# Kernel optimization log

Measured on AMD Instinct MI355X. Metric: run time of the kernel, lower is better.

Reference implementation:

```python
import jax, jax.numpy as jnp
import numpy as np

OT_REG = 0.1
OT_ITERS = 10
LN_EPS = 1e-5


def layernorm(x, g, b):
    m = jnp.mean(x, axis=-1, keepdims=True)
    v = jnp.mean((x - m) ** 2, axis=-1, keepdims=True)
    return (x - m) * jax.lax.rsqrt(v + LN_EPS) * g + b


def sinkhorn(C, epsilon, iters):
    # standard Sinkhorn: kernel exp(C/eps), alternate row/col normalization
    Q = jnp.exp(C / epsilon)  # [Na,B,La,Lb]
    def body(_, Q):
        Q = Q / jnp.sum(Q, axis=-1, keepdims=True)
        Q = Q / jnp.sum(Q, axis=-2, keepdims=True)
        return Q
    return jax.lax.fori_loop(0, iters, body, Q)


def setup_inputs() -> dict:
    key = jax.random.key(0)
    ks = jax.random.split(key, 16)
    Na, La, B, Lb, Din, H = 32, 32, 64, 32, 768, 768
    s = 0.02
    return {
        "entity_cls": jax.random.normal(ks[0], (Na, Din), jnp.float32),
        "entity_tokens": jax.random.normal(ks[1], (Na, La, Din), jnp.float32),
        "mention_cls": jax.random.normal(ks[2], (B, Din), jnp.float32),
        "mention_tokens": jax.random.normal(ks[3], (B, Lb, Din), jnp.float32),
        "Wq": jax.random.normal(ks[4], (Din, H), jnp.float32) * s,
        "bq": jnp.zeros((H,), jnp.float32),
        "Wk": jax.random.normal(ks[5], (Din, H), jnp.float32) * s,
        "bk": jnp.zeros((H,), jnp.float32),
        "Wv": jax.random.normal(ks[6], (Din, H), jnp.float32) * s,
        "bv": jnp.zeros((H,), jnp.float32),
        "ln1_g": jnp.ones((H,), jnp.float32),
        "ln1_b": jnp.zeros((H,), jnp.float32),
        "Wcls": jax.random.normal(ks[7], (Din, H), jnp.float32) * s,
        "bcls": jnp.zeros((H,), jnp.float32),
        "Wsp": jax.random.normal(ks[8], (H, 1), jnp.float32) * s,
        "bsp": jnp.zeros((1,), jnp.float32),
        "ln2_g": jnp.ones((H,), jnp.float32),
        "ln2_b": jnp.zeros((H,), jnp.float32),
    }


def reference(entity_cls, entity_tokens, mention_cls, mention_tokens,
              Wq, bq, Wk, bk, Wv, bv, ln1_g, ln1_b,
              Wcls, bcls, Wsp, bsp, ln2_g, ln2_b):
    # projections
    q = entity_tokens @ Wq + bq      # [Na,La,H]
    k = mention_tokens @ Wk + bk     # [B,Lb,H]
    v = mention_tokens @ Wv + bv     # [B,Lb,H]

    # cross-batch cosine similarity: [Na,B,La,Lb]
    qn = q / jnp.maximum(jnp.linalg.norm(q, axis=-1, keepdims=True), 1e-8)
    kn = k / jnp.maximum(jnp.linalg.norm(k, axis=-1, keepdims=True), 1e-8)
    C = jnp.einsum('aid,bjd->abij', qn, kn)

    # Sinkhorn on detached cost (torch uses C.detach())
    T = sinkhorn(jax.lax.stop_gradient(C), OT_REG, OT_ITERS)
    # F.normalize(dim=-1): L2 normalize last dim
    T = T / jnp.maximum(jnp.linalg.norm(T, axis=-1, keepdims=True), 1e-12)

    # attention + residual + layernorm: [Na,B,La,H]
    attended = jnp.einsum('abij,bjd->abid', T, v) + q[:, None, :, :]
    attended = layernorm(attended, ln1_g, ln1_b)

    # softpool over token dim (-2)
    w = jax.nn.softmax(attended @ Wsp + bsp, axis=-2)   # [Na,B,La,1]
    pooled = jnp.sum(attended * w, axis=-2)             # [Na,B,H]
    context = layernorm(pooled, ln2_g, ln2_b)

    # matching scores
    ecls = entity_cls @ Wcls + bcls                     # [Na,H]
    g2l = jnp.sum(ecls[:, None, :] * context, axis=-1)  # [Na,B]
    g2l = g2l.T                                         # [B,Na]
    g2g = mention_cls @ entity_cls.T                    # [B,Na]
    return (g2l + g2g) * 0.5
```

## Files before the change

### kernel.cpp

```cpp
#include <hip/hip_runtime.h>
#include <math.h>


typedef __attribute__((ext_vector_type(8))) short bfrag8;
typedef __attribute__((ext_vector_type(4))) float f32x4;

__device__ __forceinline__ unsigned short f2bf(float x) {
  union { float f; unsigned u; } v; v.f = x;
  unsigned r = v.u + 0x7fffu + ((v.u >> 16) & 1u);
  return (unsigned short)(r >> 16);
}

__global__ __launch_bounds__(256) void prep_kernel(
    const float* __restrict__ a0, const float* __restrict__ a1, const float* __restrict__ a2,
    unsigned short* __restrict__ o0, unsigned short* __restrict__ o1, unsigned short* __restrict__ o2,
    float* __restrict__ nrm,
    const float* __restrict__ W0, const float* __restrict__ W1,
    const float* __restrict__ W2, const float* __restrict__ W3,
    unsigned short* __restrict__ T0, unsigned short* __restrict__ T1,
    unsigned short* __restrict__ T2, unsigned short* __restrict__ T3) {
  __shared__ float t[32][33];
  int bx = blockIdx.x;
  if (bx < 2331) {
    if (bx < 2328) {
      const float* in; unsigned short* out; int i, n4;
      if (bx < 768)       { in = a0; out = o0; i = bx * 256 + threadIdx.x;          n4 = 196608; }
      else if (bx < 2304) { in = a1; out = o1; i = (bx - 768) * 256 + threadIdx.x;  n4 = 393216; }
      else                { in = a2; out = o2; i = (bx - 2304) * 256 + threadIdx.x; n4 = 6144; }
      if (i >= n4) return;
      float4 f = ((const float4*)in)[i];
      ushort4 o;
      o.x = f2bf(f.x); o.y = f2bf(f.y); o.z = f2bf(f.z); o.w = f2bf(f.w);
      ((ushort4*)out)[i] = o;
    } else {
      int i = (bx - 2328) * 256 + threadIdx.x;
      if (i < 768) ((float4*)nrm)[i] = make_float4(0.f, 0.f, 0.f, 0.f);
    }
    return;
  }
  int idx = bx - 2331;
  int z = idx / 576, r2 = idx % 576;
  int tby = r2 / 24, tbx = r2 % 24;
  const float* W = (z == 0) ? W0 : (z == 1) ? W1 : (z == 2) ? W2 : W3;
  unsigned short* O = (z == 0) ? T0 : (z == 1) ? T1 : (z == 2) ? T2 : T3;
  const int gx = tbx * 32, gy = tby * 32;
  const int tx = threadIdx.x & 31, ty = threadIdx.x >> 5;
#pragma unroll
  for (int u = 0; u < 4; ++u) {
    int row = ty + u * 8;
    t[row][tx] = W[(size_t)(gy + row) * 768 + gx + tx];
  }
  __syncthreads();
#pragma unroll
  for (int u = 0; u < 4; ++u) {
    int row = ty + u * 8;
    O[(size_t)(gx + row) * 768 + gy + tx] = f2bf(t[tx][row]);
  }
}

__global__ __launch_bounds__(256) void proj_gemm_kernel(
    const unsigned short* __restrict__ Ae, const unsigned short* __restrict__ Am,
    const unsigned short* __restrict__ Acls,
    const unsigned short* __restrict__ WqT, const unsigned short* __restrict__ WkT,
    const unsigned short* __restrict__ WvT, const unsigned short* __restrict__ WclsT,
    const float* __restrict__ bq, const float* __restrict__ bk,
    const float* __restrict__ bv, const float* __restrict__ bcls,
    unsigned short* __restrict__ qb, unsigned short* __restrict__ qT,
    unsigned short* __restrict__ kb, unsigned short* __restrict__ vT,
    float* __restrict__ ecls, float* __restrict__ iq_sq, float* __restrict__ ik_sq) {
  const int z = blockIdx.z;
  const int M = (z == 0) ? 1024 : (z == 3) ? 32 : 2048;
  const int bm = blockIdx.y * 128;
  if (bm >= M) return;
  const unsigned short* A = (z == 3) ? Acls : (z == 0) ? Ae : Am;
  const unsigned short* B = (z == 0) ? WqT : (z == 1) ? WkT : (z == 2) ? WvT : WclsT;
  const float* bias = (z == 0) ? bq : (z == 1) ? bk : (z == 2) ? bv : bcls;

  __shared__ unsigned short As[128 * 64];
  __shared__ unsigned short Bs[128 * 64];
  const int t = threadIdx.x;
  const int bn = blockIdx.x * 128;
  const int l = t & 63, w = t >> 6;
  const int wm = w & 1, wn = w >> 1;

  f32x4 acc[4][4];
#pragma unroll
  for (int mi = 0; mi < 4; ++mi)
#pragma unroll
    for (int nj = 0; nj < 4; ++nj) { f32x4 zz = {0.f, 0.f, 0.f, 0.f}; acc[mi][nj] = zz; }

  for (int k0 = 0; k0 < 768; k0 += 64) {
    __syncthreads();
#pragma unroll
    for (int u = 0; u < 4; ++u) {
      int c = t + u * 256;
      int row = c >> 3, kc = c & 7;
      int gm = bm + row; gm = gm < M ? gm : M - 1;
      int4 av = *(const int4*)(A + (size_t)gm * 768 + k0 + kc * 8);
      *(int4*)(As + row * 64 + ((kc ^ (row & 7)) * 8)) = av;
      int4 bv4 = *(const int4*)(B + (size_t)(bn + row) * 768 + k0 + kc * 8);
      *(int4*)(Bs + row * 64 + ((kc ^ (row & 7)) * 8)) = bv4;
    }
    __syncthreads();
#pragma unroll
    for (int kk = 0; kk < 2; ++kk) {
      bfrag8 af[4], bf[4];
      const int kc = kk * 4 + (l >> 4);
#pragma unroll
      for (int mi = 0; mi < 4; ++mi) {
        int arow = wm * 64 + mi * 16 + (l & 15);
        af[mi] = *(const bfrag8*)(As + arow * 64 + ((kc ^ (arow & 7)) * 8));
      }
#pragma unroll
      for (int nj = 0; nj < 4; ++nj) {
        int brow = wn * 64 + nj * 16 + (l & 15);
        bf[nj] = *(const bfrag8*)(Bs + brow * 64 + ((kc ^ (brow & 7)) * 8));
      }
#pragma unroll
      for (int mi = 0; mi < 4; ++mi)
#pragma unroll
        for (int nj = 0; nj < 4; ++nj)
          acc[mi][nj] = __builtin_amdgcn_mfma_f32_16x16x32_bf16(af[mi], bf[nj], acc[mi][nj], 0, 0, 0);
    }
  }

  const int col = l & 15, rq = l >> 4;
  float p[4][4] = {};
#pragma unroll
  for (int mi = 0; mi < 4; ++mi) {
#pragma unroll
    for (int nj = 0; nj < 4; ++nj) {
      int gn = bn + wn * 64 + nj * 16 + col;
      float bs = bias[gn];
#pragma unroll
      for (int r = 0; r < 4; ++r) {
        int gm = bm + wm * 64 + mi * 16 + rq * 4 + r;
        if (gm >= M) continue;
        float val = acc[mi][nj][r] + bs;
        if (z < 2) p[mi][r] += val * val;
        unsigned short bfv = f2bf(val);
        if (z == 0) {
          qb[(size_t)gm * 768 + gn] = bfv;
          int at = gm >> 5, j = gm & 31;
          qT[((size_t)at * 768 + gn) * 32 + j] = bfv;
        } else if (z == 1) kb[(size_t)gm * 768 + gn] = bfv;
        else if (z == 2) {
          int bb = gm >> 5, j = gm & 31;
          vT[((size_t)bb * 768 + gn) * 32 + j] = bfv;
        } else ecls[(size_t)gm * 768 + gn] = val;
      }
    }
  }
  if (z < 2) {
    float* nrm = (z == 0) ? iq_sq : ik_sq;
#pragma unroll
    for (int mi = 0; mi < 4; ++mi)
#pragma unroll
      for (int r = 0; r < 4; ++r) {
        float s = p[mi][r];
        s += __shfl_xor(s, 1); s += __shfl_xor(s, 2);
        s += __shfl_xor(s, 4); s += __shfl_xor(s, 8);
        if (col == 0) {
          int gm = bm + wm * 64 + mi * 16 + rq * 4 + r;
          atomicAdd(&nrm[gm], s);
        }
      }
  }
}

__global__ __launch_bounds__(256) void cos_attn_kernel(
    const unsigned short* __restrict__ qb, const unsigned short* __restrict__ kb,
    const float* __restrict__ iq_sq, const float* __restrict__ ik_sq,
    const unsigned short* __restrict__ qT,
    const unsigned short* __restrict__ vT,
    const float* __restrict__ ln1_g, const float* __restrict__ ln1_b,
    const float* __restrict__ Wsp, const float* __restrict__ bsp,
    const float* __restrict__ ln2_g, const float* __restrict__ ln2_b,
    const float* __restrict__ ecls,
    const float* __restrict__ entity_cls, const float* __restrict__ mention_cls,
    float* __restrict__ out) {
  __shared__ unsigned short vLds[2 * 768 * 32];
  __shared__ __align__(16) unsigned short scratch[12288];
  __shared__ float gabLds[4 * 768];
  __shared__ float gwLds[768];
  __shared__ float ldsIq[128], ldsIk[64];
  __shared__ float red[40];

  unsigned short* As = scratch;
  unsigned short* Bs = scratch + 8192;
  unsigned short* Tlds = scratch;

  const int t = threadIdx.x;
  const int l = t & 63, w = t >> 6;
  const int bm = blockIdx.y * 128, bn = blockIdx.x * 64;
  const int wm = w & 1, wn = w >> 1;
  const int cg = l & 15, rq = l >> 4;

  {
    float sgw = 0.f, sbw = 0.f, sga[4] = {}, sba[4] = {};
#pragma unroll
    for (int cc = 0; cc < 3; ++cc) {
      int h = t + cc * 256;
      float g1 = ln1_g[h], b1 = ln1_b[h], wsp = Wsp[h];
      float g2 = ln2_g[h], b2 = ln2_b[h];
      float gw = g1 * wsp;
      gwLds[h] = gw;
      sgw += gw; sbw += b1 * wsp;
#pragma unroll
      for (int aa = 0; aa < 4; ++aa) {
        float ec = ecls[(size_t)((blockIdx.y << 2) + aa) * 768 + h];
        float gab = g2 * ec;
        gabLds[aa * 768 + h] = gab;
        sga[aa] += gab; sba[aa] += b2 * ec;
      }
    }
#pragma unroll
    for (int m = 1; m < 64; m <<= 1) {
      sgw += __shfl_xor(sgw, m); sbw += __shfl_xor(sbw, m);
#pragma unroll
      for (int aa = 0; aa < 4; ++aa) { sga[aa] += __shfl_xor(sga[aa], m); sba[aa] += __shfl_xor(sba[aa], m); }
    }
    if (l == 0) {
      red[w * 10 + 0] = sgw; red[w * 10 + 1] = sbw;
#pragma unroll
      for (int aa = 0; aa < 4; ++aa) { red[w * 10 + 2 + aa] = sga[aa]; red[w * 10 + 6 + aa] = sba[aa]; }
    }
  }
  if (t < 128) ldsIq[t] = iq_sq[bm + t];
  else if (t < 192) ldsIk[t - 128] = ik_sq[bn + t - 128];

  const int4* vsrc = (const int4*)(vT + (size_t)(blockIdx.x * 2) * 768 * 32);
  int4* vdst = (int4*)vLds;

  f32x4 acc[4][2];
#pragma unroll
  for (int mi = 0; mi < 4; ++mi)
#pragma unroll
    for (int nj = 0; nj < 2; ++nj) { f32x4 zz = {0.f, 0.f, 0.f, 0.f}; acc[mi][nj] = zz; }

  for (int k0 = 0, s = 0; k0 < 768; k0 += 64, ++s) {
    __syncthreads();
#pragma unroll
    for (int u = 0; u < 4; ++u) {
      int c = t + u * 256;
      int row = c >> 3, kc = c & 7;
      int4 av = *(const int4*)(qb + (size_t)(bm + row) * 768 + k0 + kc * 8);
      *(int4*)(As + row * 64 + ((kc ^ (row & 7)) * 8)) = av;
    }
#pragma unroll
    for (int u = 0; u < 2; ++u) {
      int c = t + u * 256;
      int row = c >> 3, kc = c & 7;
      int4 bv4 = *(const int4*)(kb + (size_t)(bn + row) * 768 + k0 + kc * 8);
      *(int4*)(Bs + row * 64 + ((kc ^ (row & 7)) * 8)) = bv4;
    }
    vdst[t + (2 * s) * 256] = vsrc[t + (2 * s) * 256];
    vdst[t + (2 * s + 1) * 256] = vsrc[t + (2 * s + 1) * 256];
    __syncthreads();
#pragma unroll
    for (int kk = 0; kk < 2; ++kk) {
      bfrag8 af[4], bf[2];
      const int kc = kk * 4 + rq;
#pragma unroll
      for (int mi = 0; mi < 4; ++mi) {
        int arow = wm * 64 + mi * 16 + cg;
        af[mi] = *(const bfrag8*)(As + arow * 64 + ((kc ^ (arow & 7)) * 8));
      }
#pragma unroll
      for (int nj = 0; nj < 2; ++nj) {
        int brow = wn * 32 + nj * 16 + cg;
        bf[nj] = *(const bfrag8*)(Bs + brow * 64 + ((kc ^ (brow & 7)) * 8));
      }
#pragma unroll
      for (int mi = 0; mi < 4; ++mi)
#pragma unroll
        for (int nj = 0; nj < 2; ++nj)
          acc[mi][nj] = __builtin_amdgcn_mfma_f32_16x16x32_bf16(af[mi], bf[nj], acc[mi][nj], 0, 0, 0);
    }
  }

  float irow[4][4], icol[2];
#pragma unroll
  for (int mi = 0; mi < 4; ++mi)
#pragma unroll
    for (int r = 0; r < 4; ++r) {
      float sv = ldsIq[wm * 64 + mi * 16 + rq * 4 + r];
      irow[mi][r] = 1.0f / fmaxf(sqrtf(sv), 1e-8f);
    }
#pragma unroll
  for (int nj = 0; nj < 2; ++nj) {
    float sv = ldsIk[wn * 32 + nj * 16 + cg];
    icol[nj] = 1.0f / fmaxf(sqrtf(sv), 1e-8f);
  }
#pragma unroll
  for (int mi = 0; mi < 4; ++mi)
#pragma unroll
    for (int nj = 0; nj < 2; ++nj)
#pragma unroll
      for (int r = 0; r < 4; ++r)
        acc[mi][nj][r] = __expf(acc[mi][nj][r] * irow[mi][r] * icol[nj] * 10.0f);

  for (int it = 0; it < 10; ++it) {
#pragma unroll
    for (int mi = 0; mi < 4; ++mi)
#pragma unroll
      for (int r = 0; r < 4; ++r) {
        float rs = acc[mi][0][r] + acc[mi][1][r];
        rs += __shfl_xor(rs, 1); rs += __shfl_xor(rs, 2);
        rs += __shfl_xor(rs, 4); rs += __shfl_xor(rs, 8);
        float rinv = __builtin_amdgcn_rcpf(rs);
        acc[mi][0][r] *= rinv; acc[mi][1][r] *= rinv;
      }
#pragma unroll
    for (int ta = 0; ta < 2; ++ta)
#pragma unroll
      for (int nj = 0; nj < 2; ++nj) {
        float cs = acc[2 * ta][nj][0] + acc[2 * ta][nj][1] + acc[2 * ta][nj][2] + acc[2 * ta][nj][3]
                 + acc[2 * ta + 1][nj][0] + acc[2 * ta + 1][nj][1] + acc[2 * ta + 1][nj][2] + acc[2 * ta + 1][nj][3];
        cs += __shfl_xor(cs, 16); cs += __shfl_xor(cs, 32);
        float cinv = __builtin_amdgcn_rcpf(cs);
#pragma unroll
        for (int mi2 = 0; mi2 < 2; ++mi2)
#pragma unroll
          for (int r = 0; r < 4; ++r) acc[2 * ta + mi2][nj][r] *= cinv;
      }
  }

#pragma unroll
  for (int mi = 0; mi < 4; ++mi)
#pragma unroll
    for (int r = 0; r < 4; ++r) {
      float ss = acc[mi][0][r] * acc[mi][0][r] + acc[mi][1][r] * acc[mi][1][r];
      ss += __shfl_xor(ss, 1); ss += __shfl_xor(ss, 2);
      ss += __shfl_xor(ss, 4); ss += __shfl_xor(ss, 8);
      float tinv = 1.0f / fmaxf(sqrtf(ss), 1e-12f);
      acc[mi][0][r] *= tinv; acc[mi][1][r] *= tinv;
    }

  __syncthreads();
#pragma unroll
  for (int mi = 0; mi < 4; ++mi) {
    const int a_loc = wm * 2 + (mi >> 1);
    unsigned short* base = Tlds + ((wn * 4 + a_loc) << 10);
    const int ri0 = (mi & 1) * 16 + rq * 4;
#pragma unroll
    for (int nj = 0; nj < 2; ++nj)
#pragma unroll
      for (int r = 0; r < 4; ++r)
        base[(ri0 + r) * 32 + nj * 16 + cg] = f2bf(acc[mi][nj][r]);
  }
  __syncthreads();

  const int bl = w & 1, ah = w >> 1;
  const int b_g = (blockIdx.x << 1) + bl;
  const unsigned short* vbase = vLds + bl * 24576;

  float sgw_f = 0.f, sbw_f = 0.f, sga_f[2] = {}, sba_f[2] = {};
#pragma unroll
  for (int wv = 0; wv < 4; ++wv) {
    sgw_f += red[wv * 10 + 0]; sbw_f += red[wv * 10 + 1];
    sga_f[0] += red[wv * 10 + 2 + ah * 2]; sga_f[1] += red[wv * 10 + 3 + ah * 2];
    sba_f[0] += red[wv * 10 + 6 + ah * 2]; sba_f[1] += red[wv * 10 + 7 + ah * 2];
  }
  sbw_f += bsp[0];

  bfrag8 af[2][2], afI[2];
  const unsigned short* qTa[2];
#pragma unroll
  for (int ap = 0; ap < 2; ++ap) {
    const int a_local = ah * 2 + ap;
    qTa[ap] = qT + (size_t)((blockIdx.y << 2) + a_local) * 24576;
    const unsigned short* Tp = Tlds + ((bl * 4 + a_local) << 10);
#pragma unroll
    for (int mi = 0; mi < 2; ++mi)
      af[ap][mi] = *(const bfrag8*)(Tp + (mi * 16 + cg) * 32 + rq * 8);
  }
#pragma unroll
  for (int mi = 0; mi < 2; ++mi) {
    int row = mi * 16 + cg;
    bfrag8 fI;
#pragma unroll
    for (int u = 0; u < 8; ++u) fI[u] = (row == rq * 8 + u) ? (short)0x3F80 : (short)0;
    afI[mi] = fI;
  }

  float s1[2][2][4] = {}, s2[2][2][4] = {}, a1[2][2][4] = {};
#pragma unroll 2
  for (int nj = 0; nj < 48; ++nj) {
    int h = nj * 16 + cg;
    bfrag8 vf = *(const bfrag8*)(vbase + h * 32 + rq * 8);
    float gw = gwLds[h];
#pragma unroll
    for (int ap = 0; ap < 2; ++ap) {
      bfrag8 qf = *(const bfrag8*)(qTa[ap] + (size_t)h * 32 + rq * 8);
#pragma unroll
      for (int mi = 0; mi < 2; ++mi) {
        f32x4 zz = {0.f, 0.f, 0.f, 0.f};
        f32x4 p = __builtin_amdgcn_mfma_f32_16x16x32_bf16(af[ap][mi], vf, zz, 0, 0, 0);
        f32x4 x4 = __builtin_amdgcn_mfma_f32_16x16x32_bf16(afI[mi], qf, p, 0, 0, 0);
#pragma unroll
        for (int r = 0; r < 4; ++r) {
          float x = x4[r];
          s1[ap][mi][r] += x; s2[ap][mi][r] += x * x; a1[ap][mi][r] += x * gw;
        }
      }
    }
  }
#pragma unroll
  for (int m = 1; m < 16; m <<= 1)
#pragma unroll
    for (int ap = 0; ap < 2; ++ap)
#pragma unroll
      for (int mi = 0; mi < 2; ++mi)
#pragma unroll
        for (int r = 0; r < 4; ++r) {
          s1[ap][mi][r] += __shfl_xor(s1[ap][mi][r], m);
          s2[ap][mi][r] += __shfl_xor(s2[ap][mi][r], m);
          a1[ap][mi][r] += __shfl_xor(a1[ap][mi][r], m);
        }

  float uu[2][2][4], c0[2];
#pragma unroll
  for (int ap = 0; ap < 2; ++ap) {
    float mean[2][4], rstd[2][4], logit[2][4];
#pragma unroll
    for (int mi = 0; mi < 2; ++mi)
#pragma unroll
      for (int r = 0; r < 4; ++r) {
        float m1 = s1[ap][mi][r] * (1.0f / 768.0f);
        float var = s2[ap][mi][r] * (1.0f / 768.0f) - m1 * m1;
        float rs = rsqrtf(var + 1e-5f);
        mean[mi][r] = m1; rstd[mi][r] = rs;
        logit[mi][r] = rs * (a1[ap][mi][r] - m1 * sgw_f) + sbw_f;
      }
    float mx = logit[0][0];
#pragma unroll
    for (int mi = 0; mi < 2; ++mi)
#pragma unroll
      for (int r = 0; r < 4; ++r) mx = fmaxf(mx, logit[mi][r]);
    mx = fmaxf(mx, __shfl_xor(mx, 16)); mx = fmaxf(mx, __shfl_xor(mx, 32));
    float se = 0.f, ee[2][4];
#pragma unroll
    for (int mi = 0; mi < 2; ++mi)
#pragma unroll
      for (int r = 0; r < 4; ++r) { ee[mi][r] = __expf(logit[mi][r] - mx); se += ee[mi][r]; }
    se += __shfl_xor(se, 16); se += __shfl_xor(se, 32);
    const float sinv = __builtin_amdgcn_rcpf(se);
    float c0a = 0.f;
#pragma unroll
    for (int mi = 0; mi < 2; ++mi)
#pragma unroll
      for (int r = 0; r < 4; ++r) {
        uu[ap][mi][r] = ee[mi][r] * sinv * rstd[mi][r];
        c0a += uu[ap][mi][r] * mean[mi][r];
      }
    c0a += __shfl_xor(c0a, 16); c0a += __shfl_xor(c0a, 32);
    c0[ap] = c0a;
  }

  float ps[2] = {}, pq[2] = {}, spc[2] = {};
#pragma unroll 2
  for (int nj = 0; nj < 48; ++nj) {
    int h = nj * 16 + cg;
    bfrag8 vf = *(const bfrag8*)(vbase + h * 32 + rq * 8);
    float g1h = ln1_g[h], b1h = ln1_b[h];
#pragma unroll
    for (int ap = 0; ap < 2; ++ap) {
      bfrag8 qf = *(const bfrag8*)(qTa[ap] + (size_t)h * 32 + rq * 8);
      float pp = 0.f;
#pragma unroll
      for (int mi = 0; mi < 2; ++mi) {
        f32x4 zz = {0.f, 0.f, 0.f, 0.f};
        f32x4 p = __builtin_amdgcn_mfma_f32_16x16x32_bf16(af[ap][mi], vf, zz, 0, 0, 0);
        f32x4 x4 = __builtin_amdgcn_mfma_f32_16x16x32_bf16(afI[mi], qf, p, 0, 0, 0);
#pragma unroll
        for (int r = 0; r < 4; ++r) pp += uu[ap][mi][r] * x4[r];
      }
      pp += __shfl_xor(pp, 16); pp += __shfl_xor(pp, 32);
      float pooled = g1h * (pp - c0[ap]) + b1h;
      ps[ap] += pooled; pq[ap] += pooled * pooled;
      spc[ap] += pooled * gabLds[(ah * 2 + ap) * 768 + h];
    }
  }

#pragma unroll
  for (int ap = 0; ap < 2; ++ap) {
#pragma unroll
    for (int m = 1; m < 16; m <<= 1) {
      ps[ap] += __shfl_xor(ps[ap], m); pq[ap] += __shfl_xor(pq[ap], m); spc[ap] += __shfl_xor(spc[ap], m);
    }
    const float m2 = ps[ap] * (1.0f / 768.0f);
    const float var2 = pq[ap] * (1.0f / 768.0f) - m2 * m2;
    const float rs2 = rsqrtf(var2 + 1e-5f);
    const int a_g = (blockIdx.y << 2) + ah * 2 + ap;
    const float* ea = entity_cls + (size_t)a_g * 768;
    const float* mb = mention_cls + (size_t)b_g * 768;
    float sg = 0.f;
#pragma unroll
    for (int u = 0; u < 12; ++u) sg += mb[l * 12 + u] * ea[l * 12 + u];
#pragma unroll
    for (int m = 1; m < 64; m <<= 1) sg += __shfl_xor(sg, m);
    float tot = rs2 * (spc[ap] - m2 * sga_f[ap]) + sba_f[ap] + sg;
    if (l == 0) out[b_g * 32 + a_g] = 0.5f * tot;
  }
}

extern "C" void kernel_launch(void* const* d_in, const int* in_sizes, int n_in,
                              void* d_out, int out_size, void* d_ws, size_t ws_size,
                              hipStream_t stream) {
  const float* entity_cls     = (const float*)d_in[0];
  const float* entity_tokens  = (const float*)d_in[1];
  const float* mention_cls    = (const float*)d_in[2];
  const float* mention_tokens = (const float*)d_in[3];
  const float* Wq = (const float*)d_in[4];   const float* bq = (const float*)d_in[5];
  const float* Wk = (const float*)d_in[6];   const float* bk = (const float*)d_in[7];
  const float* Wv = (const float*)d_in[8];   const float* bv = (const float*)d_in[9];
  const float* ln1_g = (const float*)d_in[10]; const float* ln1_b = (const float*)d_in[11];
  const float* Wcls = (const float*)d_in[12];  const float* bcls = (const float*)d_in[13];
  const float* Wsp = (const float*)d_in[14];   const float* bsp = (const float*)d_in[15];
  const float* ln2_g = (const float*)d_in[16]; const float* ln2_b = (const float*)d_in[17];
  float* out = (float*)d_out;

  float* ws     = (float*)d_ws;
  float* ecls   = ws;
  float* iq_sq  = ecls + 24576;
  float* ik_sq  = iq_sq + 1024;
  unsigned short* qb = (unsigned short*)(ws + 55168);
  unsigned short* qT = qb + 786432;
  unsigned short* kb = qT + 786432;
  unsigned short* vT = kb + 1572864;
  char* R = (char*)(vT + 1572864);
  unsigned short* Ae    = (unsigned short*)R;
  unsigned short* Am    = Ae + 786432;
  unsigned short* Acls  = Am + 1572864;
  unsigned short* WqT   = Acls + 24576;
  unsigned short* WkT   = WqT + 589824;
  unsigned short* WvT   = WkT + 589824;
  unsigned short* WclsT = WvT + 589824;

  dim3 blk(256);
  prep_kernel<<<dim3(4635), blk, 0, stream>>>(
      entity_tokens, mention_tokens, entity_cls, Ae, Am, Acls, iq_sq,
      Wq, Wk, Wv, Wcls, WqT, WkT, WvT, WclsT);
  proj_gemm_kernel<<<dim3(6, 16, 4), blk, 0, stream>>>(
      Ae, Am, Acls, WqT, WkT, WvT, WclsT, bq, bk, bv, bcls,
      qb, qT, kb, vT, ecls, iq_sq, ik_sq);
  cos_attn_kernel<<<dim3(32, 8), blk, 0, stream>>>(
      qb, kb, iq_sq, ik_sq, qT, vT,
      ln1_g, ln1_b, Wsp, bsp, ln2_g, ln2_b,
      ecls, entity_cls, mention_cls, out);
}
```

Baseline: 197.4 us.

## Double cos_attn block to 512 threads, one entity-mention pair per wave

Raises the fused cosine/Sinkhorn/attention kernel from 4 to 8 waves per block while keeping the grid unchanged. Each wave now owns 32 rows (one entity) of the similarity tile instead of 64, and one (a,b) pair in the pooling phase instead of two. Tile loads, the reduction table and the launch configuration are adjusted to match. The aim is more waves in flight per CU to hide memory and MFMA latency, since large LDS use likely limits residency to one block per CU. The cost is more barrier participants and less per-wave reuse of the V fragments.

After: 179.3 us. 1.1x faster.

```diff
diff --git a/kernel.cpp b/kernel.cpp
--- a/kernel.cpp
+++ b/kernel.cpp
@@ -168,7 +168,7 @@
   }
 }
 
-__global__ __launch_bounds__(256) void cos_attn_kernel(
+__global__ __launch_bounds__(512, 2) void cos_attn_kernel(
     const unsigned short* __restrict__ qb, const unsigned short* __restrict__ kb,
     const float* __restrict__ iq_sq, const float* __restrict__ ik_sq,
     const unsigned short* __restrict__ qT,
@@ -184,7 +184,7 @@
   __shared__ float gabLds[4 * 768];
   __shared__ float gwLds[768];
   __shared__ float ldsIq[128], ldsIk[64];
-  __shared__ float red[40];
+  __shared__ float red[80];
 
   unsigned short* As = scratch;
   unsigned short* Bs = scratch + 8192;
@@ -193,14 +193,12 @@
   const int t = threadIdx.x;
   const int l = t & 63, w = t >> 6;
   const int bm = blockIdx.y * 128, bn = blockIdx.x * 64;
-  const int wm = w & 1, wn = w >> 1;
+  const int wm = w & 3, wn = w >> 2;
   const int cg = l & 15, rq = l >> 4;
 
   {
     float sgw = 0.f, sbw = 0.f, sga[4] = {}, sba[4] = {};
-#pragma unroll
-    for (int cc = 0; cc < 3; ++cc) {
-      int h = t + cc * 256;
+    for (int h = t; h < 768; h += 512) {
       float g1 = ln1_g[h], b1 = ln1_b[h], wsp = Wsp[h];
       float g2 = ln2_g[h], b2 = ln2_b[h];
       float gw = g1 * wsp;
@@ -232,38 +230,35 @@
   const int4* vsrc = (const int4*)(vT + (size_t)(blockIdx.x * 2) * 768 * 32);
   int4* vdst = (int4*)vLds;
 
-  f32x4 acc[4][2];
-#pragma unroll
-  for (int mi = 0; mi < 4; ++mi)
+  f32x4 acc[2][2];
+#pragma unroll
+  for (int mi = 0; mi < 2; ++mi)
 #pragma unroll
     for (int nj = 0; nj < 2; ++nj) { f32x4 zz = {0.f, 0.f, 0.f, 0.f}; acc[mi][nj] = zz; }
 
   for (int k0 = 0, s = 0; k0 < 768; k0 += 64, ++s) {
     __syncthreads();
 #pragma unroll
-    for (int u = 0; u < 4; ++u) {
-      int c = t + u * 256;
+    for (int u = 0; u < 2; ++u) {
+      int c = t + u * 512;
       int row = c >> 3, kc = c & 7;
       int4 av = *(const int4*)(qb + (size_t)(bm + row) * 768 + k0 + kc * 8);
       *(int4*)(As + row * 64 + ((kc ^ (row & 7)) * 8)) = av;
     }
-#pragma unroll
-    for (int u = 0; u < 2; ++u) {
-      int c = t + u * 256;
-      int row = c >> 3, kc = c & 7;
+    {
+      int row = t >> 3, kc = t & 7;
       int4 bv4 = *(const int4*)(kb + (size_t)(bn + row) * 768 + k0 + kc * 8);
       *(int4*)(Bs + row * 64 + ((kc ^ (row & 7)) * 8)) = bv4;
     }
-    vdst[t + (2 * s) * 256] = vsrc[t + (2 * s) * 256];
-    vdst[t + (2 * s + 1) * 256] = vsrc[t + (2 * s + 1) * 256];
+    vdst[t + s * 512] = vsrc[t + s * 512];
     __syncthreads();
 #pragma unroll
     for (int kk = 0; kk < 2; ++kk) {
-      bfrag8 af[4], bf[2];
+      bfrag8 af[2], bf[2];
       const int kc = kk * 4 + rq;
 #pragma unroll
-      for (int mi = 0; mi < 4; ++mi) {
-        int arow = wm * 64 + mi * 16 + cg;
+      for (int mi = 0; mi < 2; ++mi) {
+        int arow = wm * 32 + mi * 16 + cg;
         af[mi] = *(const bfrag8*)(As + arow * 64 + ((kc ^ (arow & 7)) * 8));
       }
 #pragma unroll
@@ -272,19 +267,19 @@
         bf[nj] = *(const bfrag8*)(Bs + brow * 64 + ((kc ^ (brow & 7)) * 8));
       }
 #pragma unroll
-      for (int mi = 0; mi < 4; ++mi)
+      for (int mi = 0; mi < 2; ++mi)
 #pragma unroll
         for (int nj = 0; nj < 2; ++nj)
           acc[mi][nj] = __builtin_amdgcn_mfma_f32_16x16x32_bf16(af[mi], bf[nj], acc[mi][nj], 0, 0, 0);
     }
   }
 
-  float irow[4][4], icol[2];
-#pragma unroll
-  for (int mi = 0; mi < 4; ++mi)
+  float irow[2][4], icol[2];
+#pragma unroll
+  for (int mi = 0; mi < 2; ++mi)
 #pragma unroll
     for (int r = 0; r < 4; ++r) {
-      float sv = ldsIq[wm * 64 + mi * 16 + rq * 4 + r];
+      float sv = ldsIq[wm * 32 + mi * 16 + rq * 4 + r];
       irow[mi][r] = 1.0f / fmaxf(sqrtf(sv), 1e-8f);
     }
 #pragma unroll
@@ -293,7 +288,7 @@
     icol[nj] = 1.0f / fmaxf(sqrtf(sv), 1e-8f);
   }
 #pragma unroll
-  for (int mi = 0; mi < 4; ++mi)
+  for (int mi = 0; mi < 2; ++mi)
 #pragma unroll
     for (int nj = 0; nj < 2; ++nj)
 #pragma unroll
@@ -302,7 +297,7 @@
 
   for (int it = 0; it < 10; ++it) {
 #pragma unroll
-    for (int mi = 0; mi < 4; ++mi)
+    for (int mi = 0; mi < 2; ++mi)
 #pragma unroll
       for (int r = 0; r < 4; ++r) {
         float rs = acc[mi][0][r] + acc[mi][1][r];
@@ -312,22 +307,20 @@
         acc[mi][0][r] *= rinv; acc[mi][1][r] *= rinv;
       }
 #pragma unroll
-    for (int ta = 0; ta < 2; ++ta)
-#pragma unroll
-      for (int nj = 0; nj < 2; ++nj) {
-        float cs = acc[2 * ta][nj][0] + acc[2 * ta][nj][1] + acc[2 * ta][nj][2] + acc[2 * ta][nj][3]
-                 + acc[2 * ta + 1][nj][0] + acc[2 * ta + 1][nj][1] + acc[2 * ta + 1][nj][2] + acc[2 * ta + 1][nj][3];
-        cs += __shfl_xor(cs, 16); cs += __shfl_xor(cs, 32);
-        float cinv = __builtin_amdgcn_rcpf(cs);
-#pragma unroll
-        for (int mi2 = 0; mi2 < 2; ++mi2)
-#pragma unroll
-          for (int r = 0; r < 4; ++r) acc[2 * ta + mi2][nj][r] *= cinv;
-      }
-  }
-
-#pragma unroll
-  for (int mi = 0; mi < 4; ++mi)
+    for (int nj = 0; nj < 2; ++nj) {
+      float cs = acc[0][nj][0] + acc[0][nj][1] + acc[0][nj][2] + acc[0][nj][3]
+               + acc[1][nj][0] + acc[1][nj][1] + acc[1][nj][2] + acc[1][nj][3];
+      cs += __shfl_xor(cs, 16); cs += __shfl_xor(cs, 32);
+      float cinv = __builtin_amdgcn_rcpf(cs);
+#pragma unroll
+      for (int mi = 0; mi < 2; ++mi)
+#pragma unroll
+        for (int r = 0; r < 4; ++r) acc[mi][nj][r] *= cinv;
+    }
+  }
+
+#pragma unroll
+  for (int mi = 0; mi < 2; ++mi)
 #pragma unroll
     for (int r = 0; r < 4; ++r) {
       float ss = acc[mi][0][r] * acc[mi][0][r] + acc[mi][1][r] * acc[mi][1][r];
@@ -338,45 +331,37 @@
     }
 
   __syncthreads();
-#pragma unroll
-  for (int mi = 0; mi < 4; ++mi) {
-    const int a_loc = wm * 2 + (mi >> 1);
-    unsigned short* base = Tlds + ((wn * 4 + a_loc) << 10);
-    const int ri0 = (mi & 1) * 16 + rq * 4;
-#pragma unroll
-    for (int nj = 0; nj < 2; ++nj)
-#pragma unroll
-      for (int r = 0; r < 4; ++r)
-        base[(ri0 + r) * 32 + nj * 16 + cg] = f2bf(acc[mi][nj][r]);
+  {
+    unsigned short* base = Tlds + ((wn * 4 + wm) << 10);
+#pragma unroll
+    for (int mi = 0; mi < 2; ++mi)
+#pragma unroll
+      for (int nj = 0; nj < 2; ++nj)
+#pragma unroll
+        for (int r = 0; r < 4; ++r)
+          base[(mi * 16 + rq * 4 + r) * 32 + nj * 16 + cg] = f2bf(acc[mi][nj][r]);
   }
   __syncthreads();
 
   const int bl = w & 1, ah = w >> 1;
   const int b_g = (blockIdx.x << 1) + bl;
+  const int a_g = (blockIdx.y << 2) + ah;
   const unsigned short* vbase = vLds + bl * 24576;
 
-  float sgw_f = 0.f, sbw_f = 0.f, sga_f[2] = {}, sba_f[2] = {};
-#pragma unroll
-  for (int wv = 0; wv < 4; ++wv) {
+  float sgw_f = 0.f, sbw_f = 0.f, sga_f = 0.f, sba_f = 0.f;
+#pragma unroll
+  for (int wv = 0; wv < 8; ++wv) {
     sgw_f += red[wv * 10 + 0]; sbw_f += red[wv * 10 + 1];
-    sga_f[0] += red[wv * 10 + 2 + ah * 2]; sga_f[1] += red[wv * 10 + 3 + ah * 2];
-    sba_f[0] += red[wv * 10 + 6 + ah * 2]; sba_f[1] += red[wv * 10 + 7 + ah * 2];
+    sga_f += red[wv * 10 + 2 + ah]; sba_f += red[wv * 10 + 6 + ah];
   }
   sbw_f += bsp[0];
 
-  bfrag8 af[2][2], afI[2];
-  const unsigned short* qTa[2];
-#pragma unroll
-  for (int ap = 0; ap < 2; ++ap) {
-    const int a_local = ah * 2 + ap;
-    qTa[ap] = qT + (size_t)((blockIdx.y << 2) + a_local) * 24576;
-    const unsigned short* Tp = Tlds + ((bl * 4 + a_local) << 10);
-#pragma unroll
-    for (int mi = 0; mi < 2; ++mi)
-      af[ap][mi] = *(const bfrag8*)(Tp + (mi * 16 + cg) * 32 + rq * 8);
-  }
+  const unsigned short* qTa = qT + (size_t)a_g * 24576;
+  const unsigned short* Tp = Tlds + ((bl * 4 + ah) << 10);
+  bfrag8 af[2], afI[2];
 #pragma unroll
   for (int mi = 0; mi < 2; ++mi) {
+    af[mi] = *(const bfrag8*)(Tp + (mi * 16 + cg) * 32 + rq * 8);
     int row = mi * 16 + cg;
     bfrag8 fI;
 #pragma unroll
@@ -384,54 +369,48 @@
     afI[mi] = fI;
   }
 
-  float s1[2][2][4] = {}, s2[2][2][4] = {}, a1[2][2][4] = {};
+  float s1[2][4] = {}, s2[2][4] = {}, a1[2][4] = {};
 #pragma unroll 2
   for (int nj = 0; nj < 48; ++nj) {
     int h = nj * 16 + cg;
     bfrag8 vf = *(const bfrag8*)(vbase + h * 32 + rq * 8);
+    bfrag8 qf = *(const bfrag8*)(qTa + (size_t)h * 32 + rq * 8);
     float gw = gwLds[h];
 #pragma unroll
-    for (int ap = 0; ap < 2; ++ap) {
-      bfrag8 qf = *(const bfrag8*)(qTa[ap] + (size_t)h * 32 + rq * 8);
-#pragma unroll
-      for (int mi = 0; mi < 2; ++mi) {
-        f32x4 zz = {0.f, 0.f, 0.f, 0.f};
-        f32x4 p = __builtin_amdgcn_mfma_f32_16x16x32_bf16(af[ap][mi], vf, zz, 0, 0, 0);
-        f32x4 x4 = __builtin_amdgcn_mfma_f32_16x16x32_bf16(afI[mi], qf, p, 0, 0, 0);
-#pragma unroll
-        for (int r = 0; r < 4; ++r) {
-          float x = x4[r];
-          s1[ap][mi][r] += x; s2[ap][mi][r] += x * x; a1[ap][mi][r] += x * gw;
-        }
+    for (int mi = 0; mi < 2; ++mi) {
+      f32x4 zz = {0.f, 0.f, 0.f, 0.f};
+      f32x4 p = __builtin_amdgcn_mfma_f32_16x16x32_bf16(af[mi], vf, zz, 0, 0, 0);
+      f32x4 x4 = __builtin_amdgcn_mfma_f32_16x16x32_bf16(afI[mi], qf, p, 0, 0, 0);
+#pragma unroll
+      for (int r = 0; r < 4; ++r) {
+        float x = x4[r];
+        s1[mi][r] += x; s2[mi][r] += x * x; a1[mi][r] += x * gw;
       }
     }
   }
 #pragma unroll
   for (int m = 1; m < 16; m <<= 1)
 #pragma unroll
-    for (int ap = 0; ap < 2; ++ap)
-#pragma unroll
-      for (int mi = 0; mi < 2; ++mi)
-#pragma unroll
-        for (int r = 0; r < 4; ++r) {
-          s1[ap][mi][r] += __shfl_xor(s1[ap][mi][r], m);
-          s2[ap][mi][r] += __shfl_xor(s2[ap][mi][r], m);
-          a1[ap][mi][r] += __shfl_xor(a1[ap][mi][r], m);
-        }
-
-  float uu[2][2][4], c0[2];
-#pragma unroll
-  for (int ap = 0; ap < 2; ++ap) {
+    for (int mi = 0; mi < 2; ++mi)
+#pragma unroll
+      for (int r = 0; r < 4; ++r) {
+        s1[mi][r] += __shfl_xor(s1[mi][r], m);
+        s2[mi][r] += __shfl_xor(s2[mi][r], m);
+        a1[mi][r] += __shfl_xor(a1[mi][r], m);
+      }
+
+  float uu[2][4], c0;
+  {
     float mean[2][4], rstd[2][4], logit[2][4];
 #pragma unroll
     for (int mi = 0; mi < 2; ++mi)
 #pragma unroll
       for (int r = 0; r < 4; ++r) {
-        float m1 = s1[ap][mi][r] * (1.0f / 768.0f);
-        float var = s2[ap][mi][r] * (1.0f / 768.0f) - m1 * m1;
+        float m1 = s1[mi][r] * (1.0f / 768.0f);
+        float var = s2[mi][r] * (1.0f / 768.0f) - m1 * m1;
         float rs = rsqrtf(var + 1e-5f);
         mean[mi][r] = m1; rstd[mi][r] = rs;
-        logit[mi][r] = rs * (a1[ap][mi][r] - m1 * sgw_f) + sbw_f;
+        logit[mi][r] = rs * (a1[mi][r] - m1 * sgw_f) + sbw_f;
       }
     float mx = logit[0][0];
 #pragma unroll
@@ -451,58 +430,49 @@
     for (int mi = 0; mi < 2; ++mi)
 #pragma unroll
       for (int r = 0; r < 4; ++r) {
-        uu[ap][mi][r] = ee[mi][r] * sinv * rstd[mi][r];
-        c0a += uu[ap][mi][r] * mean[mi][r];
+        uu[mi][r] = ee[mi][r] * sinv * rstd[mi][r];
+        c0a += uu[mi][r] * mean[mi][r];
       }
     c0a += __shfl_xor(c0a, 16); c0a += __shfl_xor(c0a, 32);
-    c0[ap] = c0a;
-  }
-
-  float ps[2] = {}, pq[2] = {}, spc[2] = {};
+    c0 = c0a;
+  }
+
+  float ps = 0.f, pq = 0.f, spc = 0.f;
 #pragma unroll 2
   for (int nj = 0; nj < 48; ++nj) {
     int h = nj * 16 + cg;
     bfrag8 vf = *(const bfrag8*)(vbase + h * 32 + rq * 8);
-    float g1h = ln1_g[h], b1h = ln1_b[h];
-#pragma unroll
-    for (int ap = 0; ap < 2; ++ap) {
-      bfrag8 qf = *(const bfrag8*)(qTa[ap] + (size_t)h * 32 + rq * 8);
-      float pp = 0.f;
-#pragma unroll
-      for (int mi = 0; mi < 2; ++mi) {
-        f32x4 zz = {0.f, 0.f, 0.f, 0.f};
-        f32x4 p = __builtin_amdgcn_mfma_f32_16x16x32_bf16(af[ap][mi], vf, zz, 0, 0, 0);
-        f32x4 x4 = __builtin_amdgcn_mfma_f32_16x16x32_bf16(afI[mi], qf, p, 0, 0, 0);
-#pragma unroll
-        for (int r = 0; r < 4; ++r) pp += uu[ap][mi][r] * x4[r];
-      }
-      pp += __shfl_xor(pp, 16); pp += __shfl_xor(pp, 32);
-      float pooled = g1h * (pp - c0[ap]) + b1h;
-      ps[ap] += pooled; pq[ap] += pooled * pooled;
-      spc[ap] += pooled * gabLds[(ah * 2 + ap) * 768 + h];
-    }
-  }
-
-#pragma unroll
-  for (int ap = 0; ap < 2; ++ap) {
-#pragma unroll
-    for (int m = 1; m < 16; m <<= 1) {
-      ps[ap] += __shfl_xor(ps[ap], m); pq[ap] += __shfl_xor(pq[ap], m); spc[ap] += __shfl_xor(spc[ap], m);
-    }
-    const float m2 = ps[ap] * (1.0f / 768.0f);
-    const float var2 = pq[ap] * (1.0f / 768.0f) - m2 * m2;
-    const float rs2 = rsqrtf(var2 + 1e-5f);
-    const int a_g = (blockIdx.y << 2) + ah * 2 + ap;
-    const float* ea = entity_cls + (size_t)a_g * 768;
-    const float* mb = mention_cls + (size_t)b_g * 768;
-    float sg = 0.f;
-#pragma unroll
-    for (int u = 0; u < 12; ++u) sg += mb[l * 12 + u] * ea[l * 12 + u];
-#pragma unroll
-    for (int m = 1; m < 64; m <<= 1) sg += __shfl_xor(sg, m);
-    float tot = rs2 * (spc[ap] - m2 * sga_f[ap]) + sba_f[ap] + sg;
-    if (l == 0) out[b_g * 32 + a_g] = 0.5f * tot;
-  }
+    bfrag8 qf = *(const bfrag8*)(qTa + (size_t)h * 32 + rq * 8);
+    float pp = 0.f;
+#pragma unroll
+    for (int mi = 0; mi < 2; ++mi) {
+      f32x4 zz = {0.f, 0.f, 0.f, 0.f};
+      f32x4 p = __builtin_amdgcn_mfma_f32_16x16x32_bf16(af[mi], vf, zz, 0, 0, 0);
+      f32x4 x4 = __builtin_amdgcn_mfma_f32_16x16x32_bf16(afI[mi], qf, p, 0, 0, 0);
+#pragma unroll
+      for (int r = 0; r < 4; ++r) pp += uu[mi][r] * x4[r];
+    }
+    pp += __shfl_xor(pp, 16); pp += __shfl_xor(pp, 32);
+    float pooled = ln1_g[h] * (pp - c0) + ln1_b[h];
+    ps += pooled; pq += pooled * pooled;
+    spc += pooled * gabLds[ah * 768 + h];
+  }
+#pragma unroll
+  for (int m = 1; m < 16; m <<= 1) {
+    ps += __shfl_xor(ps, m); pq += __shfl_xor(pq, m); spc += __shfl_xor(spc, m);
+  }
+  const float m2 = ps * (1.0f / 768.0f);
+  const float var2 = pq * (1.0f / 768.0f) - m2 * m2;
+  const float rs2 = rsqrtf(var2 + 1e-5f);
+  const float* ea = entity_cls + (size_t)a_g * 768;
+  const float* mb = mention_cls + (size_t)b_g * 768;
+  float sg = 0.f;
+#pragma unroll
+  for (int u = 0; u < 12; ++u) sg += mb[l * 12 + u] * ea[l * 12 + u];
+#pragma unroll
+  for (int m = 1; m < 64; m <<= 1) sg += __shfl_xor(sg, m);
+  float tot = rs2 * (spc - m2 * sga_f) + sba_f + sg;
+  if (l == 0) out[b_g * 32 + a_g] = 0.5f * tot;
 }
 
 extern "C" void kernel_launch(void* const* d_in, const int* in_sizes, int n_in,
@@ -545,7 +515,7 @@
   proj_gemm_kernel<<<dim3(6, 16, 4), blk, 0, stream>>>(
       Ae, Am, Acls, WqT, WkT, WvT, WclsT, bq, bk, bv, bcls,
       qb, qT, kb, vT, ecls, iq_sq, ik_sq);
-  cos_attn_kernel<<<dim3(32, 8), blk, 0, stream>>>(
+  cos_attn_kernel<<<dim3(32, 8), dim3(512), 0, stream>>>(
       qb, kb, iq_sq, ik_sq, qT, vT,
       ln1_g, ln1_b, Wsp, bsp, ln2_g, ln2_b,
       ecls, entity_cls, mention_cls, out);
```
